# Kernel tuning notes

Measured on AMD Instinct MI355X. Metric: run time of the kernel, lower is better.

The kernel has to match this reference:

```python
import jax, jax.numpy as jnp
import numpy as np

N_POINTS = 65536
N_ANCHORS = 1024
MAX_PTS = 512  # _MAX_POINTS_PER_BOX


def setup_inputs() -> dict:
    key = jax.random.key(0)
    k_xy, k_z, k_c, k_wl, k_h = jax.random.split(key, 5)
    # Point cloud over a 100m x 100m plot, z in [0, 10m]
    xy = jax.random.uniform(k_xy, (N_POINTS, 2), dtype=jnp.float32) * 100.0
    z = jax.random.uniform(k_z, (N_POINTS, 1), dtype=jnp.float32) * 10.0
    points = jnp.concatenate([xy, z], axis=-1)  # [N, 3]
    # Anchors: (cx, cy, cz_unused, w, l, h)
    c = jax.random.uniform(k_c, (N_ANCHORS, 2), dtype=jnp.float32) * 100.0
    cz = jnp.zeros((N_ANCHORS, 1), dtype=jnp.float32)
    wl = 1.0 + jax.random.uniform(k_wl, (N_ANCHORS, 2), dtype=jnp.float32) * 4.0
    h = 5.0 + jax.random.uniform(k_h, (N_ANCHORS, 1), dtype=jnp.float32) * 10.0
    anchors = jnp.concatenate([c, cz, wl, h], axis=-1)  # [A, 6]
    return {"points": points, "anchors": anchors, "n": MAX_PTS}


def reference(points, anchors, n):
    """Point-in-box grouping: for each anchor, gather up to n points inside its
    axis-aligned box (xy centered at cx,cy with extents w,l; z in [0,h]),
    recentered by the anchor xy. Padded to fixed size n (zeros), plus counts.
    Matches _subsample_points_batch except selection is first-n (deterministic)
    instead of randperm subsample."""
    px, py, pz = points[:, 0], points[:, 1], points[:, 2]  # [N]
    cx, cy = anchors[:, 0:1], anchors[:, 1:2]              # [A,1]
    w, l, h = anchors[:, 3:4], anchors[:, 4:5], anchors[:, 5:6]
    half_w, half_l = w * 0.5, l * 0.5
    # Dense in-box mask [A, N]
    mask = ((px[None] >= cx - half_w) & (px[None] <= cx + half_w)
            & (py[None] >= cy - half_l) & (py[None] <= cy + half_l)
            & (pz[None] >= 0.0) & (pz[None] <= h))
    counts = mask.sum(axis=1).astype(jnp.int32)            # [A]
    # top_k on 0/1 scores: ties broken by lowest index -> first n inside points
    vals, idx = jax.lax.top_k(mask.astype(jnp.float32), n)  # [A, n]
    valid = vals > 0.5                                      # [A, n]
    pts = points[idx]                                       # [A, n, 3]
    center = jnp.concatenate(
        [anchors[:, 0:2], jnp.zeros_like(anchors[:, 0:1])], axis=-1)  # [A,3]
    centered = pts - center[:, None, :]
    out = jnp.where(valid[..., None], centered, 0.0)        # [A, n, 3]
    return out, counts
```

## Files before the change

### kernel.cpp

```cpp
#include <hip/hip_runtime.h>

#define N_POINTS  65536
#define N_ANCHORS 1024
#define MAX_PTS   512
#define GX        20
#define NC        (GX * GX)
#define INV_CS    0.2f
#define NSUB      64
#define CAPS      20
#define LDS_CAP   512

#define WS_CNT    0
#define WS_BINNED 102400

__device__ __forceinline__ int cell_of(float px, float py) {
    int cx = (int)(px * INV_CS);
    int cy = (int)(py * INV_CS);
    cx = cx > GX - 1 ? GX - 1 : cx;
    cy = cy > GX - 1 ? GX - 1 : cy;
    return cy * GX + cx;
}

__global__ __launch_bounds__(256) void scatter_kernel(
    const float* __restrict__ points, int* __restrict__ cnt,
    float4* __restrict__ binned)
{
    __shared__ int lcnt[NC];
    const int b   = blockIdx.x;
    const int tid = threadIdx.x;

    for (int i = tid; i < NC; i += 256) lcnt[i] = 0;
    __syncthreads();

    const int g = b * 256 + tid;
    const float4* __restrict__ pts4 = (const float4*)points;
    const float4 A = pts4[g * 3 + 0];
    const float4 B = pts4[g * 3 + 1];
    const float4 C = pts4[g * 3 + 2];
    const float px[4] = {A.x, A.w, B.z, C.y};
    const float py[4] = {A.y, B.x, B.w, C.z};
    const float pz[4] = {A.z, B.y, C.x, C.w};
    #pragma unroll
    for (int m = 0; m < 4; ++m) {
        const int c    = cell_of(px[m], py[m]);
        const int slot = atomicAdd(&lcnt[c], 1);
        if (slot < CAPS)
            binned[(c * NSUB + b) * CAPS + slot] =
                make_float4(px[m], py[m], pz[m], __int_as_float(g * 4 + m));
    }
    __syncthreads();
    for (int i = tid; i < NC; i += 256) {
        int l = lcnt[i];
        cnt[i * NSUB + b] = l < CAPS ? l : CAPS;
    }
}

__global__ __launch_bounds__(256) void anchor_kernel(
    const float4* __restrict__ binned, const int* __restrict__ cnt,
    const float* __restrict__ anchors, float* __restrict__ out,
    float* __restrict__ counts)
{
    const int a   = blockIdx.x;
    const int tid = threadIdx.x;

    const float acx = anchors[a * 6 + 0];
    const float acy = anchors[a * 6 + 1];
    const float hw  = anchors[a * 6 + 3] * 0.5f;
    const float hl  = anchors[a * 6 + 4] * 0.5f;
    const float h   = anchors[a * 6 + 5];
    const float xmin = acx - hw, xmax = acx + hw;
    const float ymin = acy - hl, ymax = acy + hl;

    int cx0 = (int)(fmaxf(xmin, 0.0f) * INV_CS);
    int cx1 = (int)(fmaxf(xmax, 0.0f) * INV_CS);
    int cy0 = (int)(fmaxf(ymin, 0.0f) * INV_CS);
    int cy1 = (int)(fmaxf(ymax, 0.0f) * INV_CS);
    if (cx1 > GX - 1) cx1 = GX - 1;
    if (cy1 > GX - 1) cy1 = GX - 1;
    if (cx0 > GX - 1) cx0 = GX - 1;
    if (cy0 > GX - 1) cy0 = GX - 1;

    const int cell0 = cy0 * GX + cx0;
    const int cell1 = cy0 * GX + cx1;
    const int cell2 = cy1 * GX + cx0;
    const int cell3 = cy1 * GX + cx1;
    int ncells = 1;
    if (cx1 > cx0) ncells = 2;
    if (cy1 > cy0) ncells = (cx1 > cx0) ? 4 : 2;

    __shared__ int k;
    __shared__ float4 buf[LDS_CAP];

    const int q   = tid >> 6;
    const int sub = tid & (NSUB - 1);
    int len = 0, base = 0;
    if (q < ncells) {
        int ci;
        if (ncells == 1)      ci = cell0;
        else if (ncells == 2) ci = (q == 0) ? cell0 : ((cx1 > cx0) ? cell1 : cell2);
        else                  ci = (q == 0) ? cell0 : (q == 1) ? cell1
                                 : (q == 2) ? cell2 : cell3;
        len  = cnt[ci * NSUB + sub];
        base = (ci * NSUB + sub) * CAPS;
    }
    if (tid == 0) k = 0;
    __syncthreads();

    const int lane = tid & 63;
    for (int e = 0; e < len; ++e) {
        const float4 p = binned[base + e];
        const bool in = (p.x >= xmin && p.x <= xmax &&
                         p.y >= ymin && p.y <= ymax &&
                         p.z >= 0.0f && p.z <= h);
        const unsigned long long m = __ballot(in);
        if (in) {
            const int leader = __ffsll(m) - 1;
            const int nset   = __popcll(m);
            const int pre    = __popcll(m & ((1ull << lane) - 1ull));
            int wbase;
            if (lane == leader) wbase = atomicAdd(&k, nset);
            wbase = __shfl(wbase, leader);
            const int slot = wbase + pre;
            if (slot < LDS_CAP) buf[slot] = p;
        }
    }
    __syncthreads();

    const int K  = k;
    const int Kc = K < LDS_CAP ? K : LDS_CAP;

    float* __restrict__ outa = out + (size_t)a * (MAX_PTS * 3);
    for (int e = tid; e < Kc; e += 256) {
        const float4 pe = buf[e];
        const int ide = __float_as_int(pe.w);
        int rank = 0;
        for (int f = 0; f < Kc; ++f)
            rank += (__float_as_int(buf[f].w) < ide) ? 1 : 0;
        if (rank < MAX_PTS) {
            outa[rank * 3 + 0] = pe.x - acx;
            outa[rank * 3 + 1] = pe.y - acy;
            outa[rank * 3 + 2] = pe.z;
        }
    }

    if (tid == 0) counts[a] = (float)K;
}

extern "C" void kernel_launch(void* const* d_in, const int* in_sizes, int n_in,
                              void* d_out, int out_size, void* d_ws, size_t ws_size,
                              hipStream_t stream) {
    const float* points  = (const float*)d_in[0];
    const float* anchors = (const float*)d_in[1];

    float* out    = (float*)d_out;
    float* counts = (float*)d_out + (size_t)N_ANCHORS * MAX_PTS * 3;

    char* ws = (char*)d_ws;
    int*    cnt    = (int*)(ws + WS_CNT);
    float4* binned = (float4*)(ws + WS_BINNED);

    scatter_kernel<<<dim3(NSUB),      dim3(256), 0, stream>>>(points, cnt, binned);
    anchor_kernel <<<dim3(N_ANCHORS), dim3(256), 0, stream>>>(binned, cnt, anchors, out, counts);
}
```

Before: 69.29 us.

## Scatter one point per thread across more blocks and prefetch bin segments in anchor kernel

The scatter kernel now runs 256 blocks with one point per thread. Points are staged through LDS with coalesced float4 loads, and the per-block cell capacity drops to 16. The anchor kernel has each thread walk four sub-bins per cell, issues the first load of each sub-bin up front to overlap latency, and replaces the wave ballot/shuffle compaction with plain per-thread LDS atomics. This adds scatter parallelism and memory-level parallelism in the gather. The cost is four times as many count entries to read and more LDS atomic contention.

```diff
diff --git a/kernel.cpp b/kernel.cpp
--- a/kernel.cpp
+++ b/kernel.cpp
@@ -6,12 +6,12 @@
 #define GX        20
 #define NC        (GX * GX)
 #define INV_CS    0.2f
-#define NSUB      64
-#define CAPS      20
+#define NSUB      256
+#define CAPS      16
 #define LDS_CAP   512
 
 #define WS_CNT    0
-#define WS_BINNED 102400
+#define WS_BINNED 409600
 
 __device__ __forceinline__ int cell_of(float px, float py) {
     int cx = (int)(px * INV_CS);
@@ -25,29 +25,24 @@
     const float* __restrict__ points, int* __restrict__ cnt,
     float4* __restrict__ binned)
 {
-    __shared__ int lcnt[NC];
+    __shared__ int   lcnt[NC];
+    __shared__ float pstage[256 * 3];
     const int b   = blockIdx.x;
     const int tid = threadIdx.x;
 
+    if (tid < 192)
+        ((float4*)pstage)[tid] = ((const float4*)points)[b * 192 + tid];
     for (int i = tid; i < NC; i += 256) lcnt[i] = 0;
     __syncthreads();
 
-    const int g = b * 256 + tid;
-    const float4* __restrict__ pts4 = (const float4*)points;
-    const float4 A = pts4[g * 3 + 0];
-    const float4 B = pts4[g * 3 + 1];
-    const float4 C = pts4[g * 3 + 2];
-    const float px[4] = {A.x, A.w, B.z, C.y};
-    const float py[4] = {A.y, B.x, B.w, C.z};
-    const float pz[4] = {A.z, B.y, C.x, C.w};
-    #pragma unroll
-    for (int m = 0; m < 4; ++m) {
-        const int c    = cell_of(px[m], py[m]);
-        const int slot = atomicAdd(&lcnt[c], 1);
-        if (slot < CAPS)
-            binned[(c * NSUB + b) * CAPS + slot] =
-                make_float4(px[m], py[m], pz[m], __int_as_float(g * 4 + m));
-    }
+    const float px = pstage[tid * 3 + 0];
+    const float py = pstage[tid * 3 + 1];
+    const float pz = pstage[tid * 3 + 2];
+    const int c    = cell_of(px, py);
+    const int slot = atomicAdd(&lcnt[c], 1);
+    if (slot < CAPS)
+        binned[(c * NSUB + b) * CAPS + slot] =
+            make_float4(px, py, pz, __int_as_float(b * 256 + tid));
     __syncthreads();
     for (int i = tid; i < NC; i += 256) {
         int l = lcnt[i];
@@ -91,37 +86,44 @@
     __shared__ int k;
     __shared__ float4 buf[LDS_CAP];
 
-    const int q   = tid >> 6;
-    const int sub = tid & (NSUB - 1);
-    int len = 0, base = 0;
+    const int q = tid >> 6;
+    const int l = tid & 63;
+    int lens[4]  = {0, 0, 0, 0};
+    int bases[4] = {0, 0, 0, 0};
     if (q < ncells) {
         int ci;
         if (ncells == 1)      ci = cell0;
         else if (ncells == 2) ci = (q == 0) ? cell0 : ((cx1 > cx0) ? cell1 : cell2);
         else                  ci = (q == 0) ? cell0 : (q == 1) ? cell1
                                  : (q == 2) ? cell2 : cell3;
-        len  = cnt[ci * NSUB + sub];
-        base = (ci * NSUB + sub) * CAPS;
+        #pragma unroll
+        for (int r = 0; r < 4; ++r) {
+            const int seg = ci * NSUB + (l + 64 * r);
+            lens[r]  = cnt[seg];
+            bases[r] = seg * CAPS;
+        }
     }
     if (tid == 0) k = 0;
     __syncthreads();
 
-    const int lane = tid & 63;
-    for (int e = 0; e < len; ++e) {
-        const float4 p = binned[base + e];
-        const bool in = (p.x >= xmin && p.x <= xmax &&
-                         p.y >= ymin && p.y <= ymax &&
-                         p.z >= 0.0f && p.z <= h);
-        const unsigned long long m = __ballot(in);
-        if (in) {
-            const int leader = __ffsll(m) - 1;
-            const int nset   = __popcll(m);
-            const int pre    = __popcll(m & ((1ull << lane) - 1ull));
-            int wbase;
-            if (lane == leader) wbase = atomicAdd(&k, nset);
-            wbase = __shfl(wbase, leader);
-            const int slot = wbase + pre;
-            if (slot < LDS_CAP) buf[slot] = p;
+    float4 p0[4];
+    #pragma unroll
+    for (int r = 0; r < 4; ++r)
+        if (lens[r] > 0) p0[r] = binned[bases[r]];
+
+    #pragma unroll
+    for (int r = 0; r < 4; ++r) {
+        if (lens[r] <= 0) continue;
+        float4 p = p0[r];
+        for (int e = 0; ; ) {
+            if (p.x >= xmin && p.x <= xmax &&
+                p.y >= ymin && p.y <= ymax &&
+                p.z >= 0.0f && p.z <= h) {
+                const int slot = atomicAdd(&k, 1);
+                if (slot < LDS_CAP) buf[slot] = p;
+            }
+            if (++e >= lens[r]) break;
+            p = binned[bases[r] + e];
         }
     }
     __syncthreads();
```

Measured after the change: 76.99 us. +11.1%, slower.

## Fuse scatter and anchor kernels into one cooperative launch with grid sync

Applied to the files above, without the earlier changes.

Merges the binning scatter and per-anchor gather into a single cooperative kernel. The first 64 blocks bin points, then all 1024 blocks meet at a grid-wide barrier before gathering. This removes the second kernel launch and the gap between kernels. It also replaces the wave-level ballot aggregation with a per-thread LDS atomicAdd. The cost is a grid sync across all blocks, co-residency limits under launch_bounds(256,4), and more contention on the LDS atomic.

```diff
diff --git a/kernel.cpp b/kernel.cpp
--- a/kernel.cpp
+++ b/kernel.cpp
@@ -1,4 +1,7 @@
 #include <hip/hip_runtime.h>
+#include <hip/hip_cooperative_groups.h>
+
+namespace cg = cooperative_groups;
 
 #define N_POINTS  65536
 #define N_ANCHORS 1024
@@ -21,47 +24,49 @@
     return cy * GX + cx;
 }
 
-__global__ __launch_bounds__(256) void scatter_kernel(
-    const float* __restrict__ points, int* __restrict__ cnt,
-    float4* __restrict__ binned)
+__global__ __launch_bounds__(256, 4) void fused_kernel(
+    const float* __restrict__ points, const float* __restrict__ anchors,
+    float* __restrict__ out, float* __restrict__ counts,
+    int* __restrict__ cnt, float4* __restrict__ binned)
 {
-    __shared__ int lcnt[NC];
-    const int b   = blockIdx.x;
+    __shared__ int    lcnt[NC];
+    __shared__ int    k;
+    __shared__ float4 buf[LDS_CAP];
+
+    const int blk = blockIdx.x;
     const int tid = threadIdx.x;
 
-    for (int i = tid; i < NC; i += 256) lcnt[i] = 0;
-    __syncthreads();
+    if (blk < NSUB) {
+        for (int i = tid; i < NC; i += 256) lcnt[i] = 0;
+        __syncthreads();
 
-    const int g = b * 256 + tid;
-    const float4* __restrict__ pts4 = (const float4*)points;
-    const float4 A = pts4[g * 3 + 0];
-    const float4 B = pts4[g * 3 + 1];
-    const float4 C = pts4[g * 3 + 2];
-    const float px[4] = {A.x, A.w, B.z, C.y};
-    const float py[4] = {A.y, B.x, B.w, C.z};
-    const float pz[4] = {A.z, B.y, C.x, C.w};
-    #pragma unroll
-    for (int m = 0; m < 4; ++m) {
-        const int c    = cell_of(px[m], py[m]);
-        const int slot = atomicAdd(&lcnt[c], 1);
-        if (slot < CAPS)
-            binned[(c * NSUB + b) * CAPS + slot] =
-                make_float4(px[m], py[m], pz[m], __int_as_float(g * 4 + m));
+        const int g = blk * 256 + tid;
+        const float4* __restrict__ pts4 = (const float4*)points;
+        const float4 A = pts4[g * 3 + 0];
+        const float4 B = pts4[g * 3 + 1];
+        const float4 C = pts4[g * 3 + 2];
+        const float px[4] = {A.x, A.w, B.z, C.y};
+        const float py[4] = {A.y, B.x, B.w, C.z};
+        const float pz[4] = {A.z, B.y, C.x, C.w};
+        #pragma unroll
+        for (int m = 0; m < 4; ++m) {
+            const int c    = cell_of(px[m], py[m]);
+            const int slot = atomicAdd(&lcnt[c], 1);
+            if (slot < CAPS)
+                binned[(c * NSUB + blk) * CAPS + slot] =
+                    make_float4(px[m], py[m], pz[m], __int_as_float(g * 4 + m));
+        }
+        __syncthreads();
+        for (int i = tid; i < NC; i += 256) {
+            int l = lcnt[i];
+            cnt[i * NSUB + blk] = l < CAPS ? l : CAPS;
+        }
+        __threadfence();
     }
-    __syncthreads();
-    for (int i = tid; i < NC; i += 256) {
-        int l = lcnt[i];
-        cnt[i * NSUB + b] = l < CAPS ? l : CAPS;
-    }
-}
 
-__global__ __launch_bounds__(256) void anchor_kernel(
-    const float4* __restrict__ binned, const int* __restrict__ cnt,
-    const float* __restrict__ anchors, float* __restrict__ out,
-    float* __restrict__ counts)
-{
-    const int a   = blockIdx.x;
-    const int tid = threadIdx.x;
+    cg::this_grid().sync();
+
+    const int a = blk;
 
     const float acx = anchors[a * 6 + 0];
     const float acy = anchors[a * 6 + 1];
@@ -88,40 +93,30 @@
     if (cx1 > cx0) ncells = 2;
     if (cy1 > cy0) ncells = (cx1 > cx0) ? 4 : 2;
 
-    __shared__ int k;
-    __shared__ float4 buf[LDS_CAP];
-
-    const int q   = tid >> 6;
-    const int sub = tid & (NSUB - 1);
-    int len = 0, base = 0;
-    if (q < ncells) {
-        int ci;
-        if (ncells == 1)      ci = cell0;
-        else if (ncells == 2) ci = (q == 0) ? cell0 : ((cx1 > cx0) ? cell1 : cell2);
-        else                  ci = (q == 0) ? cell0 : (q == 1) ? cell1
-                                 : (q == 2) ? cell2 : cell3;
-        len  = cnt[ci * NSUB + sub];
-        base = (ci * NSUB + sub) * CAPS;
-    }
     if (tid == 0) k = 0;
     __syncthreads();
 
-    const int lane = tid & 63;
-    for (int e = 0; e < len; ++e) {
-        const float4 p = binned[base + e];
-        const bool in = (p.x >= xmin && p.x <= xmax &&
-                         p.y >= ymin && p.y <= ymax &&
-                         p.z >= 0.0f && p.z <= h);
-        const unsigned long long m = __ballot(in);
-        if (in) {
-            const int leader = __ffsll(m) - 1;
-            const int nset   = __popcll(m);
-            const int pre    = __popcll(m & ((1ull << lane) - 1ull));
-            int wbase;
-            if (lane == leader) wbase = atomicAdd(&k, nset);
-            wbase = __shfl(wbase, leader);
-            const int slot = wbase + pre;
-            if (slot < LDS_CAP) buf[slot] = p;
+    {
+        const int q   = tid >> 6;
+        const int sub = tid & (NSUB - 1);
+        int len = 0, base = 0;
+        if (q < ncells) {
+            int ci;
+            if (ncells == 1)      ci = cell0;
+            else if (ncells == 2) ci = (q == 0) ? cell0 : ((cx1 > cx0) ? cell1 : cell2);
+            else                  ci = (q == 0) ? cell0 : (q == 1) ? cell1
+                                     : (q == 2) ? cell2 : cell3;
+            len  = cnt[ci * NSUB + sub];
+            base = (ci * NSUB + sub) * CAPS;
+        }
+        for (int e = 0; e < len; ++e) {
+            const float4 p = binned[base + e];
+            if (p.x >= xmin && p.x <= xmax &&
+                p.y >= ymin && p.y <= ymax &&
+                p.z >= 0.0f && p.z <= h) {
+                const int slot = atomicAdd(&k, 1);
+                if (slot < LDS_CAP) buf[slot] = p;
+            }
         }
     }
     __syncthreads();
@@ -159,6 +154,8 @@
     int*    cnt    = (int*)(ws + WS_CNT);
     float4* binned = (float4*)(ws + WS_BINNED);
 
-    scatter_kernel<<<dim3(NSUB),      dim3(256), 0, stream>>>(points, cnt, binned);
-    anchor_kernel <<<dim3(N_ANCHORS), dim3(256), 0, stream>>>(binned, cnt, anchors, out, counts);
+    void* args[] = { (void*)&points, (void*)&anchors, (void*)&out,
+                     (void*)&counts, (void*)&cnt, (void*)&binned };
+    hipLaunchCooperativeKernel(fused_kernel, dim3(N_ANCHORS), dim3(256),
+                               args, 0, stream);
 }
```

Measured after the change: 136.5 us. 1.97x slower.
